# Optimization experiments

Measured on AMD Instinct MI355X. Metric: run time of the kernel, lower is better.

The kernel has to match this reference:

```python
import jax, jax.numpy as jnp
import numpy as np
import math

B, S, H, DK, NB = 2, 128, 4, 128, 4
D = H * DK  # 512


def setup_inputs() -> dict:
    key = jax.random.key(0)
    ks = jax.random.split(key, 24)
    g = lambda i, sh, std=1.0: jax.random.normal(ks[i], sh, jnp.float32) * std
    u = lambda i, sh: jax.random.uniform(ks[i], sh, jnp.float32)
    return {
        "x_m": g(0, (B, S, D)), "x_c": g(1, (B, S, D)),
        "b_m": g(2, (B, S, D)), "b_c": g(3, (B, S, D)),
        "bb_m": g(4, (B, NB, NB, D)), "bb_c": u(5, (B, NB, NB, D)),
        "p_m": g(6, (B, S, D)), "p_c": u(7, (B, S, D)),
        "W_xm": g(8, (3, D, H, DK), 0.02), "W_xc": g(9, (3, D, H, DK), 0.02),
        "W_bm": g(10, (3, D, H, DK), 0.02), "W_bc": g(11, (3, D, H, DK), 0.02),
        "Wq1_w": g(12, (DK, DK), 0.05), "Wq1_b": g(13, (DK,), 0.02),
        "Wq2_w": g(14, (DK, DK), 0.05), "Wq2_b": g(15, (DK,), 0.02),
        "Wk1_w": g(16, (DK, DK), 0.05), "Wk1_b": g(17, (DK,), 0.02),
        "Wk2_w": g(18, (DK, DK), 0.05), "Wk2_b": g(19, (DK,), 0.02),
        "mean_w": g(20, (D, D), 0.02), "mean_b": jnp.zeros((D,), jnp.float32),
        "cov_w": g(21, (D, D), 0.02), "cov_b": jnp.zeros((D,), jnp.float32),
        "ln_w": jnp.ones((D,), jnp.float32), "ln_b": jnp.zeros((D,), jnp.float32),
        "b_seq": jax.random.randint(ks[22], (B, S), 0, NB),
    }


def _elu1(x):
    return jax.nn.elu(x) + 1.0


def _tri_sagp(m1, m2, m3, c1, c2, c3):
    # fuse three diagonal Gaussians by product-of-Gaussians (precision-weighted)
    eps = 1e-24
    p1 = 1.0 / jnp.clip(c1, eps)
    p2 = 1.0 / jnp.clip(c2, eps)
    p3 = 1.0 / jnp.clip(c3, eps)
    c = 1.0 / (p1 + p2 + p3)
    return c * (m1 * p1 + m2 * p2 + m3 * p3), c


def _ln(x, w, b):
    m = jnp.mean(x, -1, keepdims=True)
    v = jnp.mean((x - m) ** 2, -1, keepdims=True)
    return (x - m) / jnp.sqrt(v + 1e-12) * w + b


def _forward(x_m, x_c, b_m, b_c, bb_m, bb_c, p_m, p_c,
             W_xm, W_xc, W_bm, W_bc,
             Wq1_w, Wq1_b, Wq2_w, Wq2_b, Wk1_w, Wk1_b, Wk2_w, Wk2_b,
             mean_w, mean_b, cov_w, cov_b, ln_w, ln_b, b_seq):
    Bb, Ss, Dd = x_m.shape
    Hh, Dk = W_xm.shape[2], W_xm.shape[3]
    proj = lambda x, w: jnp.einsum('bnd,dhk->bhnk', x, w)
    q1 = proj(x_m, W_xm[0]) + proj(b_m, W_bm[0])
    k1 = proj(x_m, W_xm[1]) + proj(b_m, W_bm[1])
    v1 = proj(x_m, W_xm[2]) + proj(b_m, W_bm[2])
    q2 = _elu1(proj(x_c, W_xc[0]) + proj(b_c, W_bc[0]))
    k2 = _elu1(proj(x_c, W_xc[1]) + proj(b_c, W_bc[1]))
    v2 = _elu1(proj(x_c, W_xc[2]) + proj(b_c, W_bc[2]))
    nb = bb_m.shape[1]
    # [B,NB,NB,D] -> [B,H,NB,NB,DK]
    bbm = bb_m.reshape(Bb, nb, nb, Hh, Dk).transpose(0, 3, 1, 2, 4)
    bbc = bb_c.reshape(Bb, nb, nb, Hh, Dk).transpose(0, 3, 1, 2, 4)
    # out[b,h,i,j,:] = bbm[b,h,b_seq[b,j],b_seq[b,i],:]  (matches torch advanced indexing + permute)
    gather = jax.vmap(lambda bb, seq: bb[:, seq[None, :], seq[:, None], :])
    bbm_b = gather(bbm, b_seq)  # [B,H,S,S,DK]
    bbc_b = gather(bbc, b_seq)
    pm = p_m.reshape(Bb, Ss, Hh, Dk).transpose(0, 2, 1, 3)  # [B,H,S,DK]
    pc = p_c.reshape(Bb, Ss, Hh, Dk).transpose(0, 2, 1, 3)
    lin = lambda x, w, b: x @ w.T + b
    fQm, fQc = _tri_sagp(q1[:, :, :, None, :], lin(bbm_b, Wq1_w, Wq1_b),
                         lin(pm, Wq2_w, Wq2_b)[:, :, :, None, :],
                         q2[:, :, :, None, :], bbc_b, pc[:, :, :, None, :])
    fKm, fKc = _tri_sagp(k1[:, :, None, :, :], lin(bbm_b, Wk1_w, Wk1_b),
                         lin(pm, Wk2_w, Wk2_b)[:, :, None, :, :],
                         k2[:, :, None, :, :], bbc_b, pc[:, :, None, :, :])
    eps = 1e-24
    # 2-Wasserstein^2 between diagonal Gaussians (the 1x1 matmul form reduces to this)
    w2 = jnp.sum((fQm - fKm) ** 2, -1) + jnp.sum(
        (jnp.sqrt(jnp.clip(fQc, eps)) - jnp.sqrt(jnp.clip(fKc, eps))) ** 2, -1)
    scores = -w2 / math.sqrt(Dk)  # [B,H,S,S]
    probs = jax.nn.softmax(scores, axis=-1)
    mean_ctx = jnp.einsum('bhij,bhjk->bhik', probs, v1)
    cov_ctx = jnp.einsum('bhij,bhjk->bhik', probs ** 2, v2)
    mean_ctx = mean_ctx.transpose(0, 2, 1, 3).reshape(Bb, Ss, Dd)
    cov_ctx = cov_ctx.transpose(0, 2, 1, 3).reshape(Bb, Ss, Dd)
    mean_h = _ln(mean_ctx @ mean_w.T + mean_b + x_m, ln_w, ln_b)
    cov_h = _ln(cov_ctx @ cov_w.T + cov_b + x_c, ln_w, ln_b)
    return mean_h, cov_h, probs


def reference(x_m, x_c, b_m, b_c, bb_m, bb_c, p_m, p_c,
              W_xm, W_xc, W_bm, W_bc,
              Wq1_w, Wq1_b, Wq2_w, Wq2_b, Wk1_w, Wk1_b, Wk2_w, Wk2_b,
              mean_w, mean_b, cov_w, cov_b, ln_w, ln_b, b_seq):
    return _forward(x_m, x_c, b_m, b_c, bb_m, bb_c, p_m, p_c,
                    W_xm, W_xc, W_bm, W_bc,
                    Wq1_w, Wq1_b, Wq2_w, Wq2_b, Wk1_w, Wk1_b, Wk2_w, Wk2_b,
                    mean_w, mean_b, cov_w, cov_b, ln_w, ln_b, b_seq)
```

## Files before the change

kernel.cpp:

```cpp
#include <hip/hip_runtime.h>
#include <math.h>

#define B_ 2
#define S_ 128
#define H_ 4
#define DK_ 128
#define NB_ 4
#define D_ 512
#define M_ 256

typedef __attribute__((ext_vector_type(8))) short short8;
typedef __attribute__((ext_vector_type(4))) float float4v;
typedef __attribute__((ext_vector_type(4))) unsigned short ushort4v;

__device__ __forceinline__ float elu1(float x) {
    return (x > 0.f) ? (x + 1.f) : __expf(x);
}

__device__ __forceinline__ unsigned short f2bf(float f) {
    unsigned u = __float_as_uint(f);
    unsigned r = (u + 0x7FFFu + ((u >> 16) & 1u)) >> 16;
    return (unsigned short)r;
}


union __attribute__((aligned(16))) PrepSMem {
    unsigned short tile[32][33];
    struct { float ps[2][8][128]; float wsh[2][128][33]; } c;
};

__global__ __launch_bounds__(256) void k_prep(
    const float* __restrict__ x_m, const float* __restrict__ b_m,
    const float* __restrict__ x_c, const float* __restrict__ b_c,
    const float* __restrict__ mean_w, const float* __restrict__ cov_w,
    const float* __restrict__ W_xm, const float* __restrict__ W_xc,
    const float* __restrict__ W_bm, const float* __restrict__ W_bc,
    const float* __restrict__ p_m, const float* __restrict__ bb_m,
    const float* __restrict__ Wq2, const float* __restrict__ bq2,
    const float* __restrict__ Wk2, const float* __restrict__ bk2,
    const float* __restrict__ Wq1, const float* __restrict__ bq1,
    const float* __restrict__ Wk1, const float* __restrict__ bk1,
    unsigned short* __restrict__ A_m, unsigned short* __restrict__ A_c,
    unsigned short* __restrict__ wm_bf, unsigned short* __restrict__ wc_bf,
    unsigned short* __restrict__ Wt,
    float* __restrict__ pq, float* __restrict__ pk,
    float* __restrict__ bbq, float* __restrict__ bbk)
{
    __shared__ PrepSMem sm;
    const int t = threadIdx.x;
    const int blk = blockIdx.x;
    const int u2 = t >> 7, tl = t & 127;

    {
#pragma unroll
        for (int u = 0; u < 4; ++u) {
            int cid = u * 65536 + blk * 256 + t;
            int job = cid >> 16;
            int off = (cid & 65535) * 4;
            const float* srcp;
            unsigned short* dst;
            if (job <= 1) {
                int m = off >> 10, k = off & 1023;
                if (job == 0) { srcp = (k < 512) ? (x_m + m * 512 + k) : (b_m + m * 512 + k - 512); dst = A_m; }
                else          { srcp = (k < 512) ? (x_c + m * 512 + k) : (b_c + m * 512 + k - 512); dst = A_c; }
            } else if (job == 2) { srcp = mean_w + off; dst = wm_bf; }
            else                 { srcp = cov_w + off;  dst = wc_bf; }
            float4 v = *(const float4*)srcp;
            ushort4v o;
            o.x = f2bf(v.x); o.y = f2bf(v.y); o.z = f2bf(v.z); o.w = f2bf(v.w);
            *(ushort4v*)(dst + off) = o;
        }
    }
    {
        const int tx = t & 31, ty = t >> 5;
        for (int it = 0; it < 12; ++it) {
            int tid = blk * 12 + it;
            int nt = tid & 15, kt = (tid >> 4) & 15, z = tid >> 8;
            int o = z >> 1, part = z & 1;
            const float* src;
            if (part == 0) src = (o < 3) ? (W_xm + o * 262144) : (W_xc + (o - 3) * 262144);
            else           src = (o < 3) ? (W_bm + o * 262144) : (W_bc + (o - 3) * 262144);
            __syncthreads();
#pragma unroll
            for (int u = 0; u < 4; ++u)
                sm.tile[ty + u * 8][tx] = f2bf(src[(kt * 32 + ty + u * 8) * 512 + nt * 32 + tx]);
            __syncthreads();
            unsigned short* dst = Wt + o * 524288 + part * 512;
#pragma unroll
            for (int u = 0; u < 4; ++u)
                dst[(nt * 32 + ty + u * 8) * 1024 + kt * 32 + tx] = sm.tile[tx][ty + u * 8];
        }
    }
    __syncthreads();
    if (blk < 144) {
        const int cunit = blk * 2 + u2;
        const float *src, *Wm, *bias; float* dst; int row0;
        if (cunit < 128)      { src = p_m;  Wm = Wq2; bias = bq2; dst = pq;  row0 = cunit * 8; }
        else if (cunit < 256) { src = p_m;  Wm = Wk2; bias = bk2; dst = pk;  row0 = (cunit - 128) * 8; }
        else if (cunit < 272) { src = bb_m; Wm = Wq1; bias = bq1; dst = bbq; row0 = (cunit - 256) * 8; }
        else                  { src = bb_m; Wm = Wk1; bias = bk1; dst = bbk; row0 = (cunit - 272) * 8; }

        float (*ps)[128] = sm.c.ps[u2];
        float (*wsh)[33] = sm.c.wsh[u2];
#pragma unroll
        for (int r = 0; r < 8; ++r) ps[r][tl] = src[(row0 + r) * 128 + tl];

        float acc[8];
#pragma unroll
        for (int r = 0; r < 8; ++r) acc[r] = 0.f;

        const int kc = tl & 31, kr0 = tl >> 5;
        for (int c0 = 0; c0 < 128; c0 += 32) {
            __syncthreads();
#pragma unroll 8
            for (int u = 0; u < 32; ++u)
                wsh[kr0 + u * 4][kc] = Wm[(kr0 + u * 4) * 128 + c0 + kc];
            __syncthreads();
#pragma unroll 8
            for (int k2 = 0; k2 < 32; ++k2) {
                float wvv = wsh[tl][k2];
#pragma unroll
                for (int r = 0; r < 8; ++r)
                    acc[r] = fmaf(ps[r][c0 + k2], wvv, acc[r]);
            }
        }
        float bv = bias[tl];
#pragma unroll
        for (int r = 0; r < 8; ++r) dst[(row0 + r) * 128 + tl] = acc[r] + bv;
    }
}

__global__ __launch_bounds__(256) void k_mm(
    const unsigned short* __restrict__ A_m, const unsigned short* __restrict__ A_c,
    const unsigned short* __restrict__ Wt, float* __restrict__ qkv)
{
    const int t = threadIdx.x;
    const int wid = blockIdx.x * 4 + (t >> 6);
    const int lane = t & 63;
    const int o = wid >> 9;
    const int rem = wid & 511;
    const int nt = rem & 31, mt = rem >> 5;
    const int m0 = mt * 16, n0 = nt * 16;
    const int l15 = lane & 15, quad = lane >> 4;

    const unsigned short* A = (o < 3) ? A_m : A_c;
    const unsigned short* ap = A + (m0 + l15) * 1024 + quad * 8;
    const unsigned short* bp = Wt + o * 524288 + (n0 + l15) * 1024 + quad * 8;

    float4v acc0 = {0.f, 0.f, 0.f, 0.f};
    float4v acc1 = {0.f, 0.f, 0.f, 0.f};
#pragma unroll
    for (int k0 = 0; k0 < 1024; k0 += 64) {
        short8 a0 = *(const short8*)(ap + k0);
        short8 b0 = *(const short8*)(bp + k0);
        short8 a1 = *(const short8*)(ap + k0 + 32);
        short8 b1 = *(const short8*)(bp + k0 + 32);
        acc0 = __builtin_amdgcn_mfma_f32_16x16x32_bf16(a0, b0, acc0, 0, 0, 0);
        acc1 = __builtin_amdgcn_mfma_f32_16x16x32_bf16(a1, b1, acc1, 0, 0, 0);
    }

    float* dst = qkv + o * 131072;
#pragma unroll
    for (int r = 0; r < 4; ++r) {
        float v = acc0[r] + acc1[r];
        if (o >= 3) v = elu1(v);
        dst[(m0 + quad * 4 + r) * 512 + n0 + l15] = v;
    }
}

__global__ __launch_bounds__(128) void k_fuseK(
    const float* __restrict__ qkv, const float* __restrict__ pk,
    const float* __restrict__ bbk, const float* __restrict__ bb_c,
    const float* __restrict__ p_c, const int* __restrict__ b_seq,
    float* __restrict__ fKm, float* __restrict__ fKs)
{
    const int t = threadIdx.x;
    const int j = blockIdx.x, h = blockIdx.y, b = blockIdx.z;
    const int d = h * 128 + t;
    const float eps = 1e-24f;
    const int base = (b * S_ + j) * D_ + d;
    const int sj = b_seq[b * S_ + j];

    float m1 = qkv[M_ * D_ + base];
    float c1 = qkv[4 * M_ * D_ + base];
    float m3 = pk[base];
    float c3 = p_c[base];

    float p1 = 1.f / fmaxf(c1, eps);
    float p3 = 1.f / fmaxf(c3, eps);
    float mp13 = m1 * p1 + m3 * p3;

#pragma unroll
    for (int sv = 0; sv < 4; ++sv) {
        int idx = (b * 16 + sj * 4 + sv) * 512 + d;
        float m2 = bbk[idx];
        float c2 = bb_c[idx];
        float p2 = 1.f / fmaxf(c2, eps);
        float cc = 1.f / (p1 + p2 + p3);
        int o = (((b * H_ + h) * 4 + sv) * S_ + j) * 128 + t;
        fKm[o] = cc * (mp13 + m2 * p2);
        fKs[o] = sqrtf(fmaxf(cc, eps));
    }
}

__global__ __launch_bounds__(128) void k_attn3(
    const float* __restrict__ qkv, const float* __restrict__ pq,
    const float* __restrict__ bbq, const float* __restrict__ bb_c,
    const float* __restrict__ p_c, const int* __restrict__ b_seq,
    const float* __restrict__ fKm, const float* __restrict__ fKs,
    float* __restrict__ probs_out, unsigned short* __restrict__ mctxb,
    unsigned short* __restrict__ cctxb)
{
    const int t = threadIdx.x;
    const int i = blockIdx.x, h = blockIdx.y, b = blockIdx.z;
    const float eps = 1e-24f;

    __shared__ __attribute__((aligned(16))) float qm[4 * 132];
    __shared__ __attribute__((aligned(16))) float qs[4 * 132];
    __shared__ float red[4];
    __shared__ float pr[128], pr2[128];

    const int si = b_seq[b * S_ + i];
    const int sj = b_seq[b * S_ + t];

    {
        const int d = h * 128 + t;
        const int base = (b * S_ + i) * D_ + d;
        float m1 = qkv[base];
        float c1 = qkv[3 * M_ * D_ + base];
        float m3 = pq[base];
        float c3 = p_c[base];
        float p1 = 1.f / fmaxf(c1, eps);
        float p3 = 1.f / fmaxf(c3, eps);
        float mp13 = m1 * p1 + m3 * p3;
#pragma unroll
        for (int sv = 0; sv < 4; ++sv) {
            int idx = (b * 16 + sv * 4 + si) * 512 + d;
            float m2 = bbq[idx];
            float c2 = bb_c[idx];
            float p2 = 1.f / fmaxf(c2, eps);
            float cc = 1.f / (p1 + p2 + p3);
            qm[sv * 132 + t] = cc * (mp13 + m2 * p2);
            qs[sv * 132 + t] = sqrtf(fmaxf(cc, eps));
        }
    }
    __syncthreads();

    const int krow = (((b * H_ + h) * 4 + si) * S_ + t) * 128;
    const float4* kmp = (const float4*)(fKm + krow);
    const float4* ksp = (const float4*)(fKs + krow);

    float w2 = 0.f;
#pragma unroll 4
    for (int k4 = 0; k4 < 32; ++k4) {
        float4 km = kmp[k4];
        float4 ks = ksp[k4];
        float4 m = *(const float4*)&qm[sj * 132 + k4 * 4];
        float4 s = *(const float4*)&qs[sj * 132 + k4 * 4];
        float d0 = m.x - km.x, d1 = m.y - km.y, d2 = m.z - km.z, d3 = m.w - km.w;
        float e0 = s.x - ks.x, e1 = s.y - ks.y, e2 = s.z - ks.z, e3 = s.w - ks.w;
        w2 += d0 * d0 + d1 * d1 + d2 * d2 + d3 * d3
            + e0 * e0 + e1 * e1 + e2 * e2 + e3 * e3;
    }
    float score = -w2 * 0.08838834764831845f;

    float mx = score;
#pragma unroll
    for (int off = 32; off >= 1; off >>= 1) mx = fmaxf(mx, __shfl_xor(mx, off));
    if ((t & 63) == 0) red[t >> 6] = mx;
    __syncthreads();
    mx = fmaxf(red[0], red[1]);
    float e = __expf(score - mx);
    float sm = e;
#pragma unroll
    for (int off = 32; off >= 1; off >>= 1) sm += __shfl_xor(sm, off);
    if ((t & 63) == 0) red[2 + (t >> 6)] = sm;
    __syncthreads();
    float p = e / (red[2] + red[3]);

    probs_out[((b * H_ + h) * S_ + i) * S_ + t] = p;
    pr[t] = p;
    pr2[t] = p * p;
    __syncthreads();

    const float* v1 = qkv + 2 * M_ * D_ + (b * S_) * D_ + h * 128 + t;
    const float* v2 = qkv + 5 * M_ * D_ + (b * S_) * D_ + h * 128 + t;
    float am = 0.f, ac = 0.f;
#pragma unroll 8
    for (int j = 0; j < 128; ++j) {
        am = fmaf(pr[j], v1[j * D_], am);
        ac = fmaf(pr2[j], v2[j * D_], ac);
    }
    mctxb[(b * S_ + i) * D_ + h * 128 + t] = f2bf(am);
    cctxb[(b * S_ + i) * D_ + h * 128 + t] = f2bf(ac);
}

__global__ __launch_bounds__(256) void k_fin_mm(
    const unsigned short* __restrict__ mctxb, const unsigned short* __restrict__ cctxb,
    const unsigned short* __restrict__ wm_bf, const unsigned short* __restrict__ wc_bf,
    float* __restrict__ y_m, float* __restrict__ y_c)
{
    const int t = threadIdx.x;
    const int wid = blockIdx.x * 4 + (t >> 6);
    const int lane = t & 63;
    const int mat = wid >> 9;
    const int rem = wid & 511;
    const int nt = rem & 31, mt = rem >> 5;
    const int m0 = mt * 16, n0 = nt * 16;
    const int l15 = lane & 15, quad = lane >> 4;

    const unsigned short* A = mat ? cctxb : mctxb;
    const unsigned short* Bw = mat ? wc_bf : wm_bf;
    float* y = mat ? y_c : y_m;

    const unsigned short* ap = A + (m0 + l15) * 512 + quad * 8;
    const unsigned short* bp = Bw + (n0 + l15) * 512 + quad * 8;

    float4v acc0 = {0.f, 0.f, 0.f, 0.f};
    float4v acc1 = {0.f, 0.f, 0.f, 0.f};
#pragma unroll
    for (int k0 = 0; k0 < 512; k0 += 64) {
        short8 a0 = *(const short8*)(ap + k0);
        short8 b0 = *(const short8*)(bp + k0);
        short8 a1 = *(const short8*)(ap + k0 + 32);
        short8 b1 = *(const short8*)(bp + k0 + 32);
        acc0 = __builtin_amdgcn_mfma_f32_16x16x32_bf16(a0, b0, acc0, 0, 0, 0);
        acc1 = __builtin_amdgcn_mfma_f32_16x16x32_bf16(a1, b1, acc1, 0, 0, 0);
    }
#pragma unroll
    for (int r = 0; r < 4; ++r)
        y[(m0 + quad * 4 + r) * 512 + n0 + l15] = acc0[r] + acc1[r];
}

__global__ __launch_bounds__(256) void k_ln(
    const float* __restrict__ y_m, const float* __restrict__ y_c,
    const float* __restrict__ mean_b, const float* __restrict__ cov_b,
    const float* __restrict__ x_m, const float* __restrict__ x_c,
    const float* __restrict__ ln_w, const float* __restrict__ ln_b,
    float* __restrict__ out)
{
    const int t = threadIdx.x;
    const int id = blockIdx.x;
    const int mat = id >> 8, row = id & 255;
    const float* yg = mat ? y_c : y_m;
    const float* bias = mat ? cov_b : mean_b;
    const float* res = mat ? x_c : x_m;
    const int base = row * 512;

    __shared__ float red[8];

    float y0 = yg[base + t] + bias[t] + res[base + t];
    float y1 = yg[base + 256 + t] + bias[256 + t] + res[base + 256 + t];
    float s = y0 + y1, ss = y0 * y0 + y1 * y1;
#pragma unroll
    for (int off = 32; off >= 1; off >>= 1) { s += __shfl_xor(s, off); ss += __shfl_xor(ss, off); }
    if ((t & 63) == 0) { red[t >> 6] = s; red[4 + (t >> 6)] = ss; }
    __syncthreads();
    float mu = (red[0] + red[1] + red[2] + red[3]) * (1.f / 512.f);
    float var = (red[4] + red[5] + red[6] + red[7]) * (1.f / 512.f) - mu * mu;
    float rstd = 1.f / sqrtf(var + 1e-12f);
    out[mat * 131072 + base + t] = (y0 - mu) * rstd * ln_w[t] + ln_b[t];
    out[mat * 131072 + base + 256 + t] = (y1 - mu) * rstd * ln_w[256 + t] + ln_b[256 + t];
}

extern "C" void kernel_launch(void* const* d_in, const int* in_sizes, int n_in,
                              void* d_out, int out_size, void* d_ws, size_t ws_size,
                              hipStream_t stream) {
    (void)in_sizes; (void)n_in; (void)out_size; (void)ws_size;
    const float* x_m   = (const float*)d_in[0];
    const float* x_c   = (const float*)d_in[1];
    const float* b_m   = (const float*)d_in[2];
    const float* b_c   = (const float*)d_in[3];
    const float* bb_m  = (const float*)d_in[4];
    const float* bb_c  = (const float*)d_in[5];
    const float* p_m   = (const float*)d_in[6];
    const float* p_c   = (const float*)d_in[7];
    const float* W_xm  = (const float*)d_in[8];
    const float* W_xc  = (const float*)d_in[9];
    const float* W_bm  = (const float*)d_in[10];
    const float* W_bc  = (const float*)d_in[11];
    const float* Wq1_w = (const float*)d_in[12];
    const float* Wq1_b = (const float*)d_in[13];
    const float* Wq2_w = (const float*)d_in[14];
    const float* Wq2_b = (const float*)d_in[15];
    const float* Wk1_w = (const float*)d_in[16];
    const float* Wk1_b = (const float*)d_in[17];
    const float* Wk2_w = (const float*)d_in[18];
    const float* Wk2_b = (const float*)d_in[19];
    const float* mean_w = (const float*)d_in[20];
    const float* mean_b = (const float*)d_in[21];
    const float* cov_w  = (const float*)d_in[22];
    const float* cov_b  = (const float*)d_in[23];
    const float* ln_w   = (const float*)d_in[24];
    const float* ln_b   = (const float*)d_in[25];
    const int*   b_seq  = (const int*)d_in[26];

    float* ws = (float*)d_ws;
    float* qkv = ws;
    float* pq  = ws + 786432;
    float* pk  = ws + 917504;
    float* bbq = ws + 1048576;
    float* bbk = ws + 1064960;
    float* fKm = ws + 1081344;
    float* fKs = ws + 1605632;
    float* y_m = ws + 2129920;
    float* y_c = ws + 2260992;
    unsigned short* A_m   = (unsigned short*)(ws + 2392064);
    unsigned short* A_c   = (unsigned short*)(ws + 2523136);
    unsigned short* Wt    = (unsigned short*)(ws + 2654208);
    unsigned short* wm_bf = (unsigned short*)(ws + 4227072);
    unsigned short* wc_bf = (unsigned short*)(ws + 4358144);
    unsigned short* mctxb = (unsigned short*)(ws + 4489216);
    unsigned short* cctxb = (unsigned short*)(ws + 4554752);
    float* out = (float*)d_out;

    k_prep<<<dim3(256), 256, 0, stream>>>(
        x_m, b_m, x_c, b_c, mean_w, cov_w, W_xm, W_xc, W_bm, W_bc,
        p_m, bb_m, Wq2_w, Wq2_b, Wk2_w, Wk2_b, Wq1_w, Wq1_b, Wk1_w, Wk1_b,
        A_m, A_c, wm_bf, wc_bf, Wt, pq, pk, bbq, bbk);
    k_mm<<<dim3(768), 256, 0, stream>>>(A_m, A_c, Wt, qkv);
    k_fuseK<<<dim3(128, 4, 2), 128, 0, stream>>>(
        qkv, pk, bbk, bb_c, p_c, b_seq, fKm, fKs);
    k_attn3<<<dim3(128, 4, 2), 128, 0, stream>>>(
        qkv, pq, bbq, bb_c, p_c, b_seq, fKm, fKs, out + 262144, mctxb, cctxb);
    k_fin_mm<<<dim3(256), 256, 0, stream>>>(
        mctxb, cctxb, wm_bf, wc_bf, y_m, y_c);
    k_ln<<<dim3(512), 256, 0, stream>>>(
        y_m, y_c, mean_b, cov_b, x_m, x_c, ln_w, ln_b, out);
}
```

Before: 191.1 us.

## Move small per-head linear projections from scalar FMA to MFMA in k_mm

```diff
diff --git a/kernel.cpp b/kernel.cpp
--- a/kernel.cpp
+++ b/kernel.cpp
@@ -24,11 +24,6 @@
 }
 
 
-union __attribute__((aligned(16))) PrepSMem {
-    unsigned short tile[32][33];
-    struct { float ps[2][8][128]; float wsh[2][128][33]; } c;
-};
-
 __global__ __launch_bounds__(256) void k_prep(
     const float* __restrict__ x_m, const float* __restrict__ b_m,
     const float* __restrict__ x_c, const float* __restrict__ b_c,
@@ -36,135 +31,158 @@
     const float* __restrict__ W_xm, const float* __restrict__ W_xc,
     const float* __restrict__ W_bm, const float* __restrict__ W_bc,
     const float* __restrict__ p_m, const float* __restrict__ bb_m,
-    const float* __restrict__ Wq2, const float* __restrict__ bq2,
-    const float* __restrict__ Wk2, const float* __restrict__ bk2,
-    const float* __restrict__ Wq1, const float* __restrict__ bq1,
-    const float* __restrict__ Wk1, const float* __restrict__ bk1,
+    const float* __restrict__ Wq2, const float* __restrict__ Wk2,
+    const float* __restrict__ Wq1, const float* __restrict__ Wk1,
     unsigned short* __restrict__ A_m, unsigned short* __restrict__ A_c,
     unsigned short* __restrict__ wm_bf, unsigned short* __restrict__ wc_bf,
     unsigned short* __restrict__ Wt,
-    float* __restrict__ pq, float* __restrict__ pk,
-    float* __restrict__ bbq, float* __restrict__ bbk)
-{
-    __shared__ PrepSMem sm;
+    unsigned short* __restrict__ pm_bf, unsigned short* __restrict__ bbm_bf,
+    unsigned short* __restrict__ w4_bf)
+{
+    __shared__ unsigned short tile[32][33];
     const int t = threadIdx.x;
     const int blk = blockIdx.x;
-    const int u2 = t >> 7, tl = t & 127;
-
-    {
-#pragma unroll
-        for (int u = 0; u < 4; ++u) {
-            int cid = u * 65536 + blk * 256 + t;
+    const int NBK = gridDim.x;
+
+    for (int cid = blk * 256 + t; cid < 315392; cid += NBK * 256) {
+        const float* srcp;
+        unsigned short* dstp;
+        if (cid < 262144) {
             int job = cid >> 16;
             int off = (cid & 65535) * 4;
-            const float* srcp;
-            unsigned short* dst;
             if (job <= 1) {
                 int m = off >> 10, k = off & 1023;
-                if (job == 0) { srcp = (k < 512) ? (x_m + m * 512 + k) : (b_m + m * 512 + k - 512); dst = A_m; }
-                else          { srcp = (k < 512) ? (x_c + m * 512 + k) : (b_c + m * 512 + k - 512); dst = A_c; }
-            } else if (job == 2) { srcp = mean_w + off; dst = wm_bf; }
-            else                 { srcp = cov_w + off;  dst = wc_bf; }
-            float4 v = *(const float4*)srcp;
-            ushort4v o;
-            o.x = f2bf(v.x); o.y = f2bf(v.y); o.z = f2bf(v.z); o.w = f2bf(v.w);
-            *(ushort4v*)(dst + off) = o;
-        }
-    }
-    {
-        const int tx = t & 31, ty = t >> 5;
-        for (int it = 0; it < 12; ++it) {
-            int tid = blk * 12 + it;
-            int nt = tid & 15, kt = (tid >> 4) & 15, z = tid >> 8;
-            int o = z >> 1, part = z & 1;
-            const float* src;
-            if (part == 0) src = (o < 3) ? (W_xm + o * 262144) : (W_xc + (o - 3) * 262144);
-            else           src = (o < 3) ? (W_bm + o * 262144) : (W_bc + (o - 3) * 262144);
-            __syncthreads();
-#pragma unroll
-            for (int u = 0; u < 4; ++u)
-                sm.tile[ty + u * 8][tx] = f2bf(src[(kt * 32 + ty + u * 8) * 512 + nt * 32 + tx]);
-            __syncthreads();
-            unsigned short* dst = Wt + o * 524288 + part * 512;
-#pragma unroll
-            for (int u = 0; u < 4; ++u)
-                dst[(nt * 32 + ty + u * 8) * 1024 + kt * 32 + tx] = sm.tile[tx][ty + u * 8];
-        }
-    }
-    __syncthreads();
-    if (blk < 144) {
-        const int cunit = blk * 2 + u2;
-        const float *src, *Wm, *bias; float* dst; int row0;
-        if (cunit < 128)      { src = p_m;  Wm = Wq2; bias = bq2; dst = pq;  row0 = cunit * 8; }
-        else if (cunit < 256) { src = p_m;  Wm = Wk2; bias = bk2; dst = pk;  row0 = (cunit - 128) * 8; }
-        else if (cunit < 272) { src = bb_m; Wm = Wq1; bias = bq1; dst = bbq; row0 = (cunit - 256) * 8; }
-        else                  { src = bb_m; Wm = Wk1; bias = bk1; dst = bbk; row0 = (cunit - 272) * 8; }
-
-        float (*ps)[128] = sm.c.ps[u2];
-        float (*wsh)[33] = sm.c.wsh[u2];
-#pragma unroll
-        for (int r = 0; r < 8; ++r) ps[r][tl] = src[(row0 + r) * 128 + tl];
-
-        float acc[8];
-#pragma unroll
-        for (int r = 0; r < 8; ++r) acc[r] = 0.f;
-
-        const int kc = tl & 31, kr0 = tl >> 5;
-        for (int c0 = 0; c0 < 128; c0 += 32) {
-            __syncthreads();
-#pragma unroll 8
-            for (int u = 0; u < 32; ++u)
-                wsh[kr0 + u * 4][kc] = Wm[(kr0 + u * 4) * 128 + c0 + kc];
-            __syncthreads();
-#pragma unroll 8
-            for (int k2 = 0; k2 < 32; ++k2) {
-                float wvv = wsh[tl][k2];
-#pragma unroll
-                for (int r = 0; r < 8; ++r)
-                    acc[r] = fmaf(ps[r][c0 + k2], wvv, acc[r]);
-            }
-        }
-        float bv = bias[tl];
-#pragma unroll
-        for (int r = 0; r < 8; ++r) dst[(row0 + r) * 128 + tl] = acc[r] + bv;
+                if (job == 0) { srcp = (k < 512) ? (x_m + m * 512 + k) : (b_m + m * 512 + k - 512); dstp = A_m + off; }
+                else          { srcp = (k < 512) ? (x_c + m * 512 + k) : (b_c + m * 512 + k - 512); dstp = A_c + off; }
+            } else if (job == 2) { srcp = mean_w + off; dstp = wm_bf + off; }
+            else                 { srcp = cov_w + off;  dstp = wc_bf + off; }
+        } else if (cid < 294912) {
+            int off = (cid - 262144) * 4;
+            srcp = p_m + off; dstp = pm_bf + off;
+        } else if (cid < 299008) {
+            int off = (cid - 294912) * 4;
+            srcp = bb_m + off; dstp = bbm_bf + off;
+        } else {
+            int off = (cid - 299008) * 4;
+            int seg = off >> 14;
+            const float* Ws = (seg == 0) ? Wq2 : (seg == 1) ? Wk2 : (seg == 2) ? Wq1 : Wk1;
+            srcp = Ws + (off & 16383); dstp = w4_bf + off;
+        }
+        float4 v = *(const float4*)srcp;
+        ushort4v o4;
+        o4.x = f2bf(v.x); o4.y = f2bf(v.y); o4.z = f2bf(v.z); o4.w = f2bf(v.w);
+        *(ushort4v*)dstp = o4;
+    }
+
+    const int tx = t & 31, ty = t >> 5;
+    for (int tid = blk; tid < 3072; tid += NBK) {
+        int nt = tid & 15, kt = (tid >> 4) & 15, z = tid >> 8;
+        int o = z >> 1, part = z & 1;
+        const float* src;
+        if (part == 0) src = (o < 3) ? (W_xm + o * 262144) : (W_xc + (o - 3) * 262144);
+        else           src = (o < 3) ? (W_bm + o * 262144) : (W_bc + (o - 3) * 262144);
+        __syncthreads();
+#pragma unroll
+        for (int u = 0; u < 4; ++u)
+            tile[ty + u * 8][tx] = f2bf(src[(kt * 32 + ty + u * 8) * 512 + nt * 32 + tx]);
+        __syncthreads();
+        unsigned short* dst = Wt + o * 524288 + part * 512;
+#pragma unroll
+        for (int u = 0; u < 4; ++u)
+            dst[(nt * 32 + ty + u * 8) * 1024 + kt * 32 + tx] = tile[tx][ty + u * 8];
     }
 }
 
 __global__ __launch_bounds__(256) void k_mm(
     const unsigned short* __restrict__ A_m, const unsigned short* __restrict__ A_c,
-    const unsigned short* __restrict__ Wt, float* __restrict__ qkv)
+    const unsigned short* __restrict__ Wt,
+    const unsigned short* __restrict__ pm_bf, const unsigned short* __restrict__ bbm_bf,
+    const unsigned short* __restrict__ w4_bf,
+    const float* __restrict__ bq2, const float* __restrict__ bk2,
+    const float* __restrict__ bq1, const float* __restrict__ bk1,
+    float* __restrict__ qkv, float* __restrict__ pq, float* __restrict__ pk,
+    float* __restrict__ bbq, float* __restrict__ bbk)
 {
     const int t = threadIdx.x;
     const int wid = blockIdx.x * 4 + (t >> 6);
     const int lane = t & 63;
-    const int o = wid >> 9;
-    const int rem = wid & 511;
-    const int nt = rem & 31, mt = rem >> 5;
-    const int m0 = mt * 16, n0 = nt * 16;
     const int l15 = lane & 15, quad = lane >> 4;
 
-    const unsigned short* A = (o < 3) ? A_m : A_c;
-    const unsigned short* ap = A + (m0 + l15) * 1024 + quad * 8;
-    const unsigned short* bp = Wt + o * 524288 + (n0 + l15) * 1024 + quad * 8;
-
-    float4v acc0 = {0.f, 0.f, 0.f, 0.f};
-    float4v acc1 = {0.f, 0.f, 0.f, 0.f};
-#pragma unroll
-    for (int k0 = 0; k0 < 1024; k0 += 64) {
-        short8 a0 = *(const short8*)(ap + k0);
-        short8 b0 = *(const short8*)(bp + k0);
-        short8 a1 = *(const short8*)(ap + k0 + 32);
-        short8 b1 = *(const short8*)(bp + k0 + 32);
-        acc0 = __builtin_amdgcn_mfma_f32_16x16x32_bf16(a0, b0, acc0, 0, 0, 0);
-        acc1 = __builtin_amdgcn_mfma_f32_16x16x32_bf16(a1, b1, acc1, 0, 0, 0);
-    }
-
-    float* dst = qkv + o * 131072;
-#pragma unroll
-    for (int r = 0; r < 4; ++r) {
-        float v = acc0[r] + acc1[r];
-        if (o >= 3) v = elu1(v);
-        dst[(m0 + quad * 4 + r) * 512 + n0 + l15] = v;
+    if (wid < 3072) {
+        const int o = wid >> 9;
+        const int rem = wid & 511;
+        const int nt = rem & 31, mt = rem >> 5;
+        const int m0 = mt * 16, n0 = nt * 16;
+
+        const unsigned short* A = (o < 3) ? A_m : A_c;
+        const unsigned short* ap = A + (m0 + l15) * 1024 + quad * 8;
+        const unsigned short* bp = Wt + o * 524288 + (n0 + l15) * 1024 + quad * 8;
+
+        float4v acc0 = {0.f, 0.f, 0.f, 0.f};
+        float4v acc1 = {0.f, 0.f, 0.f, 0.f};
+#pragma unroll
+        for (int k0 = 0; k0 < 1024; k0 += 64) {
+            short8 a0 = *(const short8*)(ap + k0);
+            short8 b0 = *(const short8*)(bp + k0);
+            short8 a1 = *(const short8*)(ap + k0 + 32);
+            short8 b1 = *(const short8*)(bp + k0 + 32);
+            acc0 = __builtin_amdgcn_mfma_f32_16x16x32_bf16(a0, b0, acc0, 0, 0, 0);
+            acc1 = __builtin_amdgcn_mfma_f32_16x16x32_bf16(a1, b1, acc1, 0, 0, 0);
+        }
+        float* dst = qkv + o * 131072;
+#pragma unroll
+        for (int r = 0; r < 4; ++r) {
+            float v = acc0[r] + acc1[r];
+            if (o >= 3) v = elu1(v);
+            dst[(m0 + quad * 4 + r) * 512 + n0 + l15] = v;
+        }
+    } else {
+        const unsigned short* Abf;
+        const unsigned short* Wb;
+        const float* bias;
+        float* dst;
+        int m0, n0, h;
+        if (wid < 4096) {
+            int lid = wid - 3072;
+            int sel = lid >> 9;
+            int r = lid & 511;
+            h = r >> 7;
+            int rem = r & 127;
+            m0 = (rem >> 3) * 16; n0 = (rem & 7) * 16;
+            Abf = pm_bf;
+            Wb = w4_bf + sel * 16384;
+            bias = sel ? bk2 : bq2;
+            dst = sel ? pk : pq;
+        } else {
+            int lid = wid - 4096;
+            int sel = lid >> 6;
+            int r = lid & 63;
+            h = r >> 4;
+            int rem = r & 15;
+            m0 = (rem >> 3) * 16; n0 = (rem & 7) * 16;
+            Abf = bbm_bf;
+            Wb = w4_bf + 32768 + sel * 16384;
+            bias = sel ? bk1 : bq1;
+            dst = sel ? bbk : bbq;
+        }
+        const unsigned short* ap = Abf + (m0 + l15) * 512 + h * 128 + quad * 8;
+        const unsigned short* bp = Wb + (n0 + l15) * 128 + quad * 8;
+
+        float4v acc0 = {0.f, 0.f, 0.f, 0.f};
+        float4v acc1 = {0.f, 0.f, 0.f, 0.f};
+#pragma unroll
+        for (int k0 = 0; k0 < 128; k0 += 64) {
+            short8 a0 = *(const short8*)(ap + k0);
+            short8 b0 = *(const short8*)(bp + k0);
+            short8 a1 = *(const short8*)(ap + k0 + 32);
+            short8 b1 = *(const short8*)(bp + k0 + 32);
+            acc0 = __builtin_amdgcn_mfma_f32_16x16x32_bf16(a0, b0, acc0, 0, 0, 0);
+            acc1 = __builtin_amdgcn_mfma_f32_16x16x32_bf16(a1, b1, acc1, 0, 0, 0);
+        }
+        float bv = bias[n0 + l15];
+#pragma unroll
+        for (int r = 0; r < 4; ++r)
+            dst[(m0 + quad * 4 + r) * 512 + h * 128 + n0 + l15] = acc0[r] + acc1[r] + bv;
     }
 }
 
@@ -405,20 +423,26 @@
     float* fKs = ws + 1605632;
     float* y_m = ws + 2129920;
     float* y_c = ws + 2260992;
-    unsigned short* A_m   = (unsigned short*)(ws + 2392064);
-    unsigned short* A_c   = (unsigned short*)(ws + 2523136);
-    unsigned short* Wt    = (unsigned short*)(ws + 2654208);
-    unsigned short* wm_bf = (unsigned short*)(ws + 4227072);
-    unsigned short* wc_bf = (unsigned short*)(ws + 4358144);
-    unsigned short* mctxb = (unsigned short*)(ws + 4489216);
-    unsigned short* cctxb = (unsigned short*)(ws + 4554752);
+    unsigned short* A_m    = (unsigned short*)(ws + 2392064);
+    unsigned short* A_c    = (unsigned short*)(ws + 2523136);
+    unsigned short* Wt     = (unsigned short*)(ws + 2654208);
+    unsigned short* wm_bf  = (unsigned short*)(ws + 4227072);
+    unsigned short* wc_bf  = (unsigned short*)(ws + 4358144);
+    unsigned short* mctxb  = (unsigned short*)(ws + 4489216);
+    unsigned short* cctxb  = (unsigned short*)(ws + 4554752);
+    unsigned short* pm_bf  = (unsigned short*)(ws + 4620288);
+    unsigned short* bbm_bf = (unsigned short*)(ws + 4685824);
+    unsigned short* w4_bf  = (unsigned short*)(ws + 4694016);
     float* out = (float*)d_out;
 
-    k_prep<<<dim3(256), 256, 0, stream>>>(
+    k_prep<<<dim3(768), 256, 0, stream>>>(
         x_m, b_m, x_c, b_c, mean_w, cov_w, W_xm, W_xc, W_bm, W_bc,
-        p_m, bb_m, Wq2_w, Wq2_b, Wk2_w, Wk2_b, Wq1_w, Wq1_b, Wk1_w, Wk1_b,
-        A_m, A_c, wm_bf, wc_bf, Wt, pq, pk, bbq, bbk);
-    k_mm<<<dim3(768), 256, 0, stream>>>(A_m, A_c, Wt, qkv);
+        p_m, bb_m, Wq2_w, Wk2_w, Wq1_w, Wk1_w,
+        A_m, A_c, wm_bf, wc_bf, Wt, pm_bf, bbm_bf, w4_bf);
+    k_mm<<<dim3(1056), 256, 0, stream>>>(
+        A_m, A_c, Wt, pm_bf, bbm_bf, w4_bf,
+        Wq2_b, Wk2_b, Wq1_b, Wk1_b,
+        qkv, pq, pk, bbq, bbk);
     k_fuseK<<<dim3(128, 4, 2), 128, 0, stream>>>(
         qkv, pk, bbk, bb_c, p_c, b_seq, fKm, fKs);
     k_attn3<<<dim3(128, 4, 2), 128, 0, stream>>>(
```

Measured after the change: 177.5 us. 7.1% less time.
